# Kernel tuning notes

Measured on AMD Instinct MI355X. Metric: run time of the kernel, lower is better.

The kernel has to match this reference:

```python
import jax, jax.numpy as jnp
import numpy as np

N = 32768          # number of points
K = 64             # max_num_neighbors
D = 3              # spatial dim (3x3 local frames)
R = 1.0            # radius
TARGET_DEG = 48.0  # desired mean neighborhood size


def _radius_graph_numpy(pos, r, k):
    """Padded radius neighbor search (mimics torch_cluster.radius, incl. self-loop).

    Returns (edge_src, edge_dst, num_neighbors); padded slots have src == dst so
    edge_vec = 0 and they contribute nothing to the covariance scatter.
    """
    n = pos.shape[0]
    nbr = np.full((n, k), -1, dtype=np.int64)
    r2 = r * r
    chunk = 2048
    for s in range(0, n, chunk):
        q = pos[s:s + chunk]                                   # [C, D]
        d2 = ((q[:, None, :] - pos[None, :, :]) ** 2).sum(-1)  # [C, N]
        d2m = np.where(d2 <= r2, d2, np.inf)
        idx = np.argpartition(d2m, k - 1, axis=1)[:, :k]       # k nearest candidates
        dsel = np.take_along_axis(d2m, idx, axis=1)
        nbr[s:s + chunk] = np.where(np.isfinite(dsel), idx, -1)
    num_neighbors = (nbr >= 0).sum(axis=1).astype(np.int32)
    edge_dst = np.repeat(np.arange(n, dtype=np.int64), k)
    edge_src = nbr.reshape(-1)
    edge_src = np.where(edge_src >= 0, edge_src, edge_dst)     # pad: src == dst
    return edge_src.astype(np.int32), edge_dst.astype(np.int32), num_neighbors


def setup_inputs() -> dict:
    rng = np.random.default_rng(0)
    # box size so that density * (4/3) pi r^3 ~= TARGET_DEG
    L = (N * (4.0 / 3.0) * np.pi * R ** 3 / TARGET_DEG) ** (1.0 / 3.0)
    pos = rng.uniform(0.0, L, size=(N, D)).astype(np.float32)
    edge_src, edge_dst, num_neighbors = _radius_graph_numpy(pos, R, K)
    return {
        "pos": jnp.asarray(pos),
        "edge_src": jnp.asarray(edge_src),
        "edge_dst": jnp.asarray(edge_dst),
        "num_neighbors": jnp.asarray(num_neighbors),
    }


def reference(pos, edge_src, edge_dst, num_neighbors):
    n = pos.shape[0]
    # edge_vec = pos[col] - pos[row]; padded edges (src==dst) give exact zeros
    ev = pos[edge_src] - pos[edge_dst]                         # [E, 3]
    outer = ev[:, :, None] * ev[:, None, :]                    # [E, 3, 3]
    cov = jax.ops.segment_sum(outer, edge_dst, num_segments=n)  # [N, 3, 3]

    no_nbr = num_neighbors <= 1                                # self-loop only
    # replace degenerate (zero) covariances with a distinct-eigenvalue matrix so
    # eigh is well-defined; these rows are zeroed afterwards (exceptional 'zero').
    safe = jnp.diag(jnp.arange(1.0, D + 1.0, dtype=pos.dtype))
    cov = jnp.where(no_nbr[:, None, None], safe, cov)

    _, vecs = jnp.linalg.eigh(cov)                             # [N, 3, 3] columns = eigvecs
    frames = vecs.transpose(0, 2, 1)                           # rows = eigvecs
    frames = jnp.where(no_nbr[:, None, None], 0.0, frames)
    return frames


if __name__ == "__main__":
    out = reference(**setup_inputs())
    print(out.shape, out.dtype)
```

## Files before the change

### kernel.cpp

```cpp
#include <hip/hip_runtime.h>
#include <math.h>


#pragma clang fp contract(off)

#define EPS_F32    5.9604645e-8f
#define SAFMIN_F32 1.17549435e-38f

__device__ __forceinline__ float lapy2f(float x, float y) {
#pragma clang fp contract(off)
  float xa = fabsf(x), ya = fabsf(y);
  float w = fmaxf(xa, ya);
  float z = fminf(xa, ya);
  if (z == 0.0f) return w;
  float t = z / w;
  return w * sqrtf(1.0f + t * t);
}

__device__ __forceinline__ void slartgf(float f, float g, float* c, float* s, float* r) {
#pragma clang fp contract(off)
  const float safmin = SAFMIN_F32;
  const float safmax = 8.50705917e37f;
  const float rtmin  = 1.08420217e-19f;
  const float rtmax  = 6.52530446e18f;
  if (g == 0.0f) { *c = 1.0f; *s = 0.0f; *r = f; return; }
  if (f == 0.0f) { *c = 0.0f; *s = copysignf(1.0f, g); *r = fabsf(g); return; }
  float f1 = fabsf(f), g1 = fabsf(g);
  if (f1 > rtmin && f1 < rtmax && g1 > rtmin && g1 < rtmax) {
    float d = sqrtf(f * f + g * g);
    *c = f1 / d;
    *r = copysignf(d, f);
    *s = g / (*r);
  } else {
    float u  = fminf(safmax, fmaxf(safmin, fmaxf(f1, g1)));
    float fs = f / u, gs = g / u;
    float d  = sqrtf(fs * fs + gs * gs);
    *c = fabsf(fs) / d;
    float rr = copysignf(d, f);
    *s = gs / rr;
    *r = rr * u;
  }
}

__device__ __forceinline__ void slaev2f(float a, float b, float c,
                                        float* rt1, float* rt2,
                                        float* cs1, float* sn1) {
#pragma clang fp contract(off)
  float sm  = a + c;
  float df  = a - c;
  float adf = fabsf(df);
  float tb  = b + b;
  float ab  = fabsf(tb);
  float acmx, acmn;
  if (fabsf(a) > fabsf(c)) { acmx = a; acmn = c; } else { acmx = c; acmn = a; }
  float rt;
  if (adf > ab)      { float t = ab / adf; rt = adf * sqrtf(1.0f + t * t); }
  else if (adf < ab) { float t = adf / ab; rt = ab  * sqrtf(1.0f + t * t); }
  else               { rt = ab * sqrtf(2.0f); }
  int sgn1;
  if (sm < 0.0f) {
    *rt1 = 0.5f * (sm - rt); sgn1 = -1;
    *rt2 = (acmx / *rt1) * acmn - (b / *rt1) * b;
  } else if (sm > 0.0f) {
    *rt1 = 0.5f * (sm + rt); sgn1 = 1;
    *rt2 = (acmx / *rt1) * acmn - (b / *rt1) * b;
  } else {
    *rt1 = 0.5f * rt; *rt2 = -0.5f * rt; sgn1 = 1;
  }
  int sgn2; float cs;
  if (df >= 0.0f) { cs = df + rt; sgn2 = 1; }
  else            { cs = df - rt; sgn2 = -1; }
  float acs = fabsf(cs);
  if (acs > ab) {
    float ct = -tb / cs;
    *sn1 = 1.0f / sqrtf(1.0f + ct * ct);
    *cs1 = ct * (*sn1);
  } else {
    if (ab == 0.0f) { *cs1 = 1.0f; *sn1 = 0.0f; }
    else {
      float tn = -cs / tb;
      *cs1 = 1.0f / sqrtf(1.0f + tn * tn);
      *sn1 = tn * (*cs1);
    }
  }
  if (sgn1 == sgn2) { float tn = *cs1; *cs1 = -(*sn1); *sn1 = tn; }
}

__device__ void eig_frames_reg(float c00, float c01, float c02,
                               float c11, float c12, float c22,
                               float* __restrict__ o) {
#pragma clang fp contract(off)
  float d1, d2, d3, e1, e2, tau1, v2;
  {
    float a11 = c00, a21 = c01, a31 = c02, a22 = c11, a32 = c12, a33 = c22;
    float xnorm = fabsf(a31);
    if (xnorm == 0.0f) {
      tau1 = 0.0f; v2 = 0.0f;
      d1 = a11; d2 = a22; d3 = a33;
      e1 = a21; e2 = a32;
    } else {
      float py2  = lapy2f(a21, xnorm);
      float beta = -copysignf(py2, a21);
      tau1 = (beta - a21) / beta;
      v2   = a31 * (1.0f / (a21 - beta));
      float t2 = a32 * v2;
      float w1 = __builtin_fmaf(tau1, t2, tau1 * a22);
      float w2 = __builtin_fmaf(tau1 * v2, a33, tau1 * a32);
      float dot = __builtin_fmaf(v2, w2, w1);
      float ac = (-0.5f * tau1) * dot;
      w1 = w1 + ac;
      w2 = __builtin_fmaf(ac, v2, w2);
      float A11 = a22 - w1;
      A11 = A11 - w1;
      float A21 = a32 - w2;
      A21 = __builtin_fmaf(-w1, v2, A21);
      float A33 = __builtin_fmaf(-v2, w2, a33);
      A33 = __builtin_fmaf(-w2, v2, A33);
      d1 = a11; d2 = A11; d3 = A33;
      e1 = beta; e2 = A21;
    }
  }

  float z11 = 1.0f, z12 = 0.0f, z13 = 0.0f;
  float z21 = 0.0f, z22 = 1.0f, z23 = 0.0f;
  float z31 = 0.0f, z32 = 0.0f, z33 = 1.0f;
  float wc0, wc1, ws0, ws1;

#define DGET(i)    ((i) == 1 ? d1 : (i) == 2 ? d2 : d3)
#define DSET(i,v)  do { float _t = (v); if ((i) == 1) d1 = _t; else if ((i) == 2) d2 = _t; else d3 = _t; } while (0)
#define EGET(i)    ((i) == 1 ? e1 : e2)
#define ESET(i,v)  do { float _t = (v); if ((i) == 1) e1 = _t; else e2 = _t; } while (0)
#define ZGETC(r,c) ((r) == 1 ? ((c) == 1 ? z11 : (c) == 2 ? z12 : z13) \
                  : (r) == 2 ? ((c) == 1 ? z21 : (c) == 2 ? z22 : z23) \
                  :            ((c) == 1 ? z31 : (c) == 2 ? z32 : z33))
#define ZSETC(r,c,v) do { float _t = (v); \
    if ((r) == 1)      { if ((c) == 1) z11 = _t; else if ((c) == 2) z12 = _t; else z13 = _t; } \
    else if ((r) == 2) { if ((c) == 1) z21 = _t; else if ((c) == 2) z22 = _t; else z23 = _t; } \
    else               { if ((c) == 1) z31 = _t; else if ((c) == 2) z32 = _t; else z33 = _t; } } while (0)

  {
    const float eps    = EPS_F32;
    const float eps2   = eps * eps;
    const float safmin = SAFMIN_F32;
    const float ssfmax = sqrtf(8.50705917e37f) / 3.0f;
    const float ssfmin = sqrtf(safmin) / eps2;

    int   l1, l, m, lsv, lend, lendsv, iscale;
    const int nmaxit = 90;
    int   jtot = 0;
    float anorm, p, g, r, rt1, rt2, rc, rs, f, b, t;

    l1 = 1;

L10:
    if (l1 > 3) goto L160;
    if (l1 > 1) ESET(l1 - 1, 0.0f);
    if (l1 <= 2) {
      for (m = l1; m <= 2; m++) {
        float tst = fabsf(EGET(m));
        if (tst == 0.0f) goto L30;
        if (tst <= (sqrtf(fabsf(DGET(m))) * sqrtf(fabsf(DGET(m + 1)))) * eps) {
          ESET(m, 0.0f);
          goto L30;
        }
      }
    }
    m = 3;
L30:
    l = l1; lsv = l; lend = m; lendsv = lend; l1 = m + 1;
    if (lend == l) goto L10;

    anorm = 0.0f;
    for (int q = l; q <= lend; q++)     anorm = fmaxf(anorm, fabsf(DGET(q)));
    for (int q = l; q <= lend - 1; q++) anorm = fmaxf(anorm, fabsf(EGET(q)));
    iscale = 0;
    if (anorm == 0.0f) goto L10;
    if (anorm > ssfmax) {
      iscale = 1;
      float sc = ssfmax / anorm;
      for (int q = l; q <= lend; q++)     DSET(q, DGET(q) * sc);
      for (int q = l; q <= lend - 1; q++) ESET(q, EGET(q) * sc);
    } else if (anorm < ssfmin) {
      iscale = 2;
      float sc = ssfmin / anorm;
      for (int q = l; q <= lend; q++)     DSET(q, DGET(q) * sc);
      for (int q = l; q <= lend - 1; q++) ESET(q, EGET(q) * sc);
    }

    if (fabsf(DGET(lend)) < fabsf(DGET(l))) { lend = lsv; l = lendsv; }

    if (lend > l) {
L40:
      if (l != lend) {
        if (l == 1) {
          float tst = e1 * e1;
          if (tst <= (eps2 * fabsf(d1)) * fabsf(d2) + safmin) { m = 1; goto L60; }
        }
        if (lend == 3) {
          float tst = e2 * e2;
          if (tst <= (eps2 * fabsf(d2)) * fabsf(d3) + safmin) { m = 2; goto L60; }
        }
      }
      m = lend;
L60:
      if (m < lend) ESET(m, 0.0f);
      p = DGET(l);
      if (m == l) goto L80;
      if (m == l + 1) {
        if (l == 1) {
          slaev2f(d1, e1, d2, &rt1, &rt2, &rc, &rs);
          t = z12; z12 = rc * t - rs * z11; z11 = rs * t + rc * z11;
          t = z22; z22 = rc * t - rs * z21; z21 = rs * t + rc * z21;
          t = z32; z32 = rc * t - rs * z31; z31 = rs * t + rc * z31;
          d1 = rt1; d2 = rt2; e1 = 0.0f;
        } else {
          slaev2f(d2, e2, d3, &rt1, &rt2, &rc, &rs);
          t = z13; z13 = rc * t - rs * z12; z12 = rs * t + rc * z12;
          t = z23; z23 = rc * t - rs * z22; z22 = rs * t + rc * z22;
          t = z33; z33 = rc * t - rs * z32; z32 = rs * t + rc * z32;
          d2 = rt1; d3 = rt2; e2 = 0.0f;
        }
        l += 2;
        if (l <= lend) goto L40;
        goto L140;
      }
      if (jtot == nmaxit) goto L140;
      jtot++;
      g = (d2 - p) / (2.0f * e1);
      r = lapy2f(g, 1.0f);
      g = d3 - p + (e1 / (g + copysignf(r, g)));
      rs = 1.0f; rc = 1.0f; p = 0.0f;
      f = rs * e2;
      b = rc * e2;
      slartgf(g, f, &rc, &rs, &r);
      g = d3 - p;
      r = (d2 - g) * rs + 2.0f * rc * b;
      p = rs * r;
      d3 = g + p;
      g = rc * r - b;
      wc1 = rc; ws1 = -rs;
      f = rs * e1;
      b = rc * e1;
      slartgf(g, f, &rc, &rs, &r);
      e2 = r;
      g = d2 - p;
      r = (d1 - g) * rs + 2.0f * rc * b;
      p = rs * r;
      d2 = g + p;
      g = rc * r - b;
      wc0 = rc; ws0 = -rs;
      if (wc1 != 1.0f || ws1 != 0.0f) {
        t = z13; z13 = wc1 * t - ws1 * z12; z12 = ws1 * t + wc1 * z12;
        t = z23; z23 = wc1 * t - ws1 * z22; z22 = ws1 * t + wc1 * z22;
        t = z33; z33 = wc1 * t - ws1 * z32; z32 = ws1 * t + wc1 * z32;
      }
      if (wc0 != 1.0f || ws0 != 0.0f) {
        t = z12; z12 = wc0 * t - ws0 * z11; z11 = ws0 * t + wc0 * z11;
        t = z22; z22 = wc0 * t - ws0 * z21; z21 = ws0 * t + wc0 * z21;
        t = z32; z32 = wc0 * t - ws0 * z31; z31 = ws0 * t + wc0 * z31;
      }
      d1 = d1 - p;
      e1 = g;
      goto L40;
L80:
      DSET(l, p);
      l++;
      if (l <= lend) goto L40;
      goto L140;
    } else {
L90:
      if (l != lend) {
        if (l == 3) {
          float tst = e2 * e2;
          if (tst <= (eps2 * fabsf(d3)) * fabsf(d2) + safmin) { m = 3; goto L110; }
        }
        if (lend == 1) {
          float tst = e1 * e1;
          if (tst <= (eps2 * fabsf(d2)) * fabsf(d1) + safmin) { m = 2; goto L110; }
        }
      }
      m = lend;
L110:
      if (m > lend) ESET(m - 1, 0.0f);
      p = DGET(l);
      if (m == l) goto L130;
      if (m == l - 1) {
        if (l == 2) {
          slaev2f(d1, e1, d2, &rt1, &rt2, &rc, &rs);
          t = z12; z12 = rc * t - rs * z11; z11 = rs * t + rc * z11;
          t = z22; z22 = rc * t - rs * z21; z21 = rs * t + rc * z21;
          t = z32; z32 = rc * t - rs * z31; z31 = rs * t + rc * z31;
          d1 = rt1; d2 = rt2; e1 = 0.0f;
        } else {
          slaev2f(d2, e2, d3, &rt1, &rt2, &rc, &rs);
          t = z13; z13 = rc * t - rs * z12; z12 = rs * t + rc * z12;
          t = z23; z23 = rc * t - rs * z22; z22 = rs * t + rc * z22;
          t = z33; z33 = rc * t - rs * z32; z32 = rs * t + rc * z32;
          d2 = rt1; d3 = rt2; e2 = 0.0f;
        }
        l -= 2;
        if (l >= lend) goto L90;
        goto L140;
      }
      if (jtot == nmaxit) goto L140;
      jtot++;
      g = (d2 - p) / (2.0f * e2);
      r = lapy2f(g, 1.0f);
      g = d1 - p + (e2 / (g + copysignf(r, g)));
      rs = 1.0f; rc = 1.0f; p = 0.0f;
      f = rs * e1;
      b = rc * e1;
      slartgf(g, f, &rc, &rs, &r);
      g = d1 - p;
      r = (d2 - g) * rs + 2.0f * rc * b;
      p = rs * r;
      d1 = g + p;
      g = rc * r - b;
      wc0 = rc; ws0 = rs;
      f = rs * e2;
      b = rc * e2;
      slartgf(g, f, &rc, &rs, &r);
      e1 = r;
      g = d2 - p;
      r = (d3 - g) * rs + 2.0f * rc * b;
      p = rs * r;
      d2 = g + p;
      g = rc * r - b;
      wc1 = rc; ws1 = rs;
      if (wc0 != 1.0f || ws0 != 0.0f) {
        t = z12; z12 = wc0 * t - ws0 * z11; z11 = ws0 * t + wc0 * z11;
        t = z22; z22 = wc0 * t - ws0 * z21; z21 = ws0 * t + wc0 * z21;
        t = z32; z32 = wc0 * t - ws0 * z31; z31 = ws0 * t + wc0 * z31;
      }
      if (wc1 != 1.0f || ws1 != 0.0f) {
        t = z13; z13 = wc1 * t - ws1 * z12; z12 = ws1 * t + wc1 * z12;
        t = z23; z23 = wc1 * t - ws1 * z22; z22 = ws1 * t + wc1 * z22;
        t = z33; z33 = wc1 * t - ws1 * z32; z32 = ws1 * t + wc1 * z32;
      }
      d3 = d3 - p;
      e2 = g;
      goto L90;
L130:
      DSET(l, p);
      l--;
      if (l >= lend) goto L90;
      goto L140;
    }

L140:
    if (iscale == 1) {
      float sc = anorm / ssfmax;
      for (int q = lsv; q <= lendsv; q++)     DSET(q, DGET(q) * sc);
      for (int q = lsv; q <= lendsv - 1; q++) ESET(q, EGET(q) * sc);
    } else if (iscale == 2) {
      float sc = anorm / ssfmin;
      for (int q = lsv; q <= lendsv; q++)     DSET(q, DGET(q) * sc);
      for (int q = lsv; q <= lendsv - 1; q++) ESET(q, EGET(q) * sc);
    }
    if (jtot < nmaxit) goto L10;
    goto L160;

L160:
    for (int ii = 2; ii <= 3; ii++) {
      int i = ii - 1, kk = i;
      p = DGET(i);
      for (int j = ii; j <= 3; j++) {
        if (DGET(j) < p) { kk = j; p = DGET(j); }
      }
      if (kk != i) {
        DSET(kk, DGET(i));
        DSET(i, p);
        #pragma unroll
        for (int row = 1; row <= 3; row++) {
          float tt = ZGETC(row, i);
          ZSETC(row, i, ZGETC(row, kk));
          ZSETC(row, kk, tt);
        }
      }
    }
  }

#undef DGET
#undef DSET
#undef EGET
#undef ESET
#undef ZGETC
#undef ZSETC

  if (tau1 != 0.0f) {
    {
      float z2 = z21, z3 = z31;
      float w = z2 + z3 * v2;
      float t = tau1 * w;
      z21 = __builtin_fmaf(-tau1, w, z2);
      z31 = __builtin_fmaf(v2, -t, z3);
    }
    {
      float z2 = z22, z3 = z32;
      float w = z2 + z3 * v2;
      float t = tau1 * w;
      z22 = __builtin_fmaf(-tau1, w, z2);
      z32 = __builtin_fmaf(v2, -t, z3);
    }
    {
      float z2 = z23, z3 = z33;
      float w = z2 + z3 * v2;
      float t = tau1 * w;
      z23 = __builtin_fmaf(-tau1, w, z2);
      z33 = __builtin_fmaf(v2, -t, z3);
    }
  }

  o[0] = z11; o[1] = z21; o[2] = z31;
  o[3] = z12; o[4] = z22; o[5] = z32;
  o[6] = z13; o[7] = z23; o[8] = z33;
}

#define NODES_PER_BLOCK 64
#define NODE_STRIDE     193

struct __attribute__((aligned(4))) f3 { float x, y, z; };

__global__ void __launch_bounds__(256)
pca_frames_tiled_kernel(const float* __restrict__ pos,
                        const int*   __restrict__ esrc,
                        const int*   __restrict__ nn,
                        float*       __restrict__ out,
                        int n)
{
#pragma clang fp contract(off)
  __shared__ float sev[NODES_PER_BLOCK * NODE_STRIDE];

  const int tid   = threadIdx.x;
  const int node0 = blockIdx.x * NODES_PER_BLOCK;

  const int ebase = blockIdx.x * (NODES_PER_BLOCK * 64);
  #pragma unroll
  for (int q = 0; q < (NODES_PER_BLOCK * 64) / 256; ++q) {
    int eb  = q * 256 + tid;
    int n_b = eb >> 6;
    int j   = eb & 63;
    int i   = node0 + n_b;
    int s   = esrc[ebase + eb];
    f3 ps   = *reinterpret_cast<const f3*>(pos + 3 * s);
    float dx = ps.x - pos[3 * i + 0];
    float dy = ps.y - pos[3 * i + 1];
    float dz = ps.z - pos[3 * i + 2];
    float* row = sev + n_b * NODE_STRIDE + 3 * j;
    row[0] = dx;
    row[1] = dy;
    row[2] = dz;
  }

  __syncthreads();

  if (tid < 64) {
    int i = node0 + tid;
    float* o = out + (size_t)i * 9;

    if (nn[i] <= 1) {
      #pragma unroll
      for (int j = 0; j < 9; ++j) o[j] = 0.0f;
      return;
    }

    const float* row = sev + tid * NODE_STRIDE;
    float c00 = 0.0f, c01 = 0.0f, c02 = 0.0f, c11 = 0.0f, c12 = 0.0f, c22 = 0.0f;
    for (int j = 0; j < 64; ++j) {
      float dx = row[3 * j + 0];
      float dy = row[3 * j + 1];
      float dz = row[3 * j + 2];
      c00 = c00 + dx * dx;
      c01 = c01 + dx * dy;
      c02 = c02 + dx * dz;
      c11 = c11 + dy * dy;
      c12 = c12 + dy * dz;
      c22 = c22 + dz * dz;
    }

    eig_frames_reg(c00, c01, c02, c11, c12, c22, o);
  }
}

__global__ void __launch_bounds__(64)
pca_frames_fused_kernel(const float* __restrict__ pos,
                        const int*   __restrict__ esrc,
                        const int*   __restrict__ nn,
                        float*       __restrict__ out,
                        int n, int k)
{
#pragma clang fp contract(off)
  int i = blockIdx.x * blockDim.x + threadIdx.x;
  if (i >= n) return;
  float* o = out + (size_t)i * 9;

  if (nn[i] <= 1) {
    #pragma unroll
    for (int j = 0; j < 9; ++j) o[j] = 0.0f;
    return;
  }

  float px = pos[3 * i + 0], py = pos[3 * i + 1], pz = pos[3 * i + 2];
  float c00 = 0.0f, c01 = 0.0f, c02 = 0.0f, c11 = 0.0f, c12 = 0.0f, c22 = 0.0f;
  const int* ep = esrc + (size_t)i * k;
  for (int j = 0; j < k; ++j) {
    int sidx = ep[j];
    float dx = pos[3 * sidx + 0] - px;
    float dy = pos[3 * sidx + 1] - py;
    float dz = pos[3 * sidx + 2] - pz;
    c00 = c00 + dx * dx;
    c01 = c01 + dx * dy;
    c02 = c02 + dx * dz;
    c11 = c11 + dy * dy;
    c12 = c12 + dy * dz;
    c22 = c22 + dz * dz;
  }

  eig_frames_reg(c00, c01, c02, c11, c12, c22, o);
}

extern "C" void kernel_launch(void* const* d_in, const int* in_sizes, int n_in,
                              void* d_out, int out_size, void* d_ws, size_t ws_size,
                              hipStream_t stream) {
  const float* pos  = (const float*)d_in[0];
  const int*   esrc = (const int*)d_in[1];
  const int*   nn   = (const int*)d_in[3];
  float*       out  = (float*)d_out;

  int n = in_sizes[0] / 3;
  if (n <= 0) return;
  int k = in_sizes[1] / n;

  if (k == 64 && (n % NODES_PER_BLOCK) == 0) {
    hipLaunchKernelGGL(pca_frames_tiled_kernel, dim3(n / NODES_PER_BLOCK),
                       dim3(256), 0, stream, pos, esrc, nn, out, n);
  } else {
    const int block = 64;
    hipLaunchKernelGGL(pca_frames_fused_kernel, dim3((n + block - 1) / block),
                       dim3(block), 0, stream, pos, esrc, nn, out, n, k);
  }
}
```

Before: 95.36 us.

## Restructure QL/QR eigen iteration as a wave-uniform state machine to cut divergence

Replaces the goto-based LAPACK ssteqr port with an explicit state machine looping until no lane in the wavefront is active. The QL and QR branches are merged into one sweep body by index mirroring (dirQL), so lanes that take different directions now run the same code instead of serialised divergent paths. The cost is extra selects, per-iteration __any wave votes, and register pressure from the mirrored indexing.

```diff
diff --git a/kernel.cpp b/kernel.cpp
--- a/kernel.cpp
+++ b/kernel.cpp
@@ -86,9 +86,17 @@
   if (sgn1 == sgn2) { float tn = *cs1; *cs1 = -(*sn1); *sn1 = tn; }
 }
 
-__device__ void eig_frames_reg(float c00, float c01, float c02,
-                               float c11, float c12, float c22,
-                               float* __restrict__ o) {
+#define ST_SEG   0
+#define ST_CHK   1
+#define ST_X21   2
+#define ST_X32   3
+#define ST_SWP   4
+#define ST_RESC  5
+#define ST_DONE  6
+
+__device__ void eig_frames_sm(float c00, float c01, float c02,
+                              float c11, float c12, float c22,
+                              float* __restrict__ o) {
 #pragma clang fp contract(off)
   float d1, d2, d3, e1, e2, tau1, v2;
   {
@@ -124,12 +132,15 @@
   float z11 = 1.0f, z12 = 0.0f, z13 = 0.0f;
   float z21 = 0.0f, z22 = 1.0f, z23 = 0.0f;
   float z31 = 0.0f, z32 = 0.0f, z33 = 1.0f;
-  float wc0, wc1, ws0, ws1;
 
 #define DGET(i)    ((i) == 1 ? d1 : (i) == 2 ? d2 : d3)
 #define DSET(i,v)  do { float _t = (v); if ((i) == 1) d1 = _t; else if ((i) == 2) d2 = _t; else d3 = _t; } while (0)
 #define EGET(i)    ((i) == 1 ? e1 : e2)
 #define ESET(i,v)  do { float _t = (v); if ((i) == 1) e1 = _t; else e2 = _t; } while (0)
+#define AGET(i)    DGET(dirQL ? (i) : 4 - (i))
+#define ASET(i,v)  DSET(dirQL ? (i) : 4 - (i), v)
+#define BGET(i)    EGET(dirQL ? (i) : 3 - (i))
+#define BSET(i,v)  ESET(dirQL ? (i) : 3 - (i), v)
 #define ZGETC(r,c) ((r) == 1 ? ((c) == 1 ? z11 : (c) == 2 ? z12 : z13) \
                   : (r) == 2 ? ((c) == 1 ? z21 : (c) == 2 ? z22 : z23) \
                   :            ((c) == 1 ? z31 : (c) == 2 ? z32 : z33))
@@ -138,229 +149,217 @@
     else if ((r) == 2) { if ((c) == 1) z21 = _t; else if ((c) == 2) z22 = _t; else z23 = _t; } \
     else               { if ((c) == 1) z31 = _t; else if ((c) == 2) z32 = _t; else z33 = _t; } } while (0)
 
+  const float eps    = EPS_F32;
+  const float eps2   = eps * eps;
+  const float safmin = SAFMIN_F32;
+  const float ssfmax = sqrtf(8.50705917e37f) / 3.0f;
+  const float ssfmin = sqrtf(safmin) / eps2;
+  const int   nmaxit = 90;
+
+  int   st = ST_SEG, nst = ST_CHK;
+  int   l1 = 1, lm = 1, lendm = 1, lsv = 1, lendsv = 1, iscale = 0, jtot = 0;
+  bool  dirQL = true;
+  float anorm = 0.0f, p = 0.0f;
+
+  for (int it = 0; it < 600; ++it) {
+    if (!__any(st != ST_DONE)) break;
+
+    if (st == ST_SEG) {
+      for (int pass = 0; pass < 4 && st == ST_SEG; ++pass) {
+        if (l1 > 3) { st = ST_DONE; break; }
+        if (l1 > 1) ESET(l1 - 1, 0.0f);
+        int m = 3;
+        {
+          bool found = false;
+          if (l1 <= 2) {
+            for (int mi = l1; mi <= 2 && !found; mi++) {
+              float tst = fabsf(EGET(mi));
+              if (tst == 0.0f) { m = mi; found = true; }
+              else if (tst <= (sqrtf(fabsf(DGET(mi))) * sqrtf(fabsf(DGET(mi + 1)))) * eps) {
+                ESET(mi, 0.0f); m = mi; found = true;
+              }
+            }
+          }
+        }
+        int l = l1; lsv = l; int lend = m; lendsv = lend; l1 = m + 1;
+        if (lend == l) continue;
+        anorm = 0.0f;
+        for (int q = l; q <= lend; q++)     anorm = fmaxf(anorm, fabsf(DGET(q)));
+        for (int q = l; q <= lend - 1; q++) anorm = fmaxf(anorm, fabsf(EGET(q)));
+        iscale = 0;
+        if (anorm == 0.0f) continue;
+        if (anorm > ssfmax) {
+          iscale = 1;
+          float sc = ssfmax / anorm;
+          for (int q = l; q <= lend; q++)     DSET(q, DGET(q) * sc);
+          for (int q = l; q <= lend - 1; q++) ESET(q, EGET(q) * sc);
+        } else if (anorm < ssfmin) {
+          iscale = 2;
+          float sc = ssfmin / anorm;
+          for (int q = l; q <= lend; q++)     DSET(q, DGET(q) * sc);
+          for (int q = l; q <= lend - 1; q++) ESET(q, EGET(q) * sc);
+        }
+        if (fabsf(DGET(lend)) < fabsf(DGET(l))) { int tt = l; l = lend; lend = tt; }
+        dirQL = (lend > l);
+        lm    = dirQL ? l : 4 - l;
+        lendm = dirQL ? lend : 4 - lend;
+        st = ST_CHK;
+      }
+    }
+
+    if (st == ST_CHK) {
+      int mm = lendm;
+      {
+        bool found = false;
+        if (lm != lendm) {
+          if (lm == 1) {
+            float bb = BGET(1);
+            float tst = bb * bb;
+            if (tst <= (eps2 * fabsf(AGET(1))) * fabsf(AGET(2)) + safmin) { mm = 1; found = true; }
+          }
+          if (!found && lendm == 3) {
+            float bb = BGET(2);
+            float tst = bb * bb;
+            if (tst <= (eps2 * fabsf(AGET(2))) * fabsf(AGET(3)) + safmin) { mm = 2; found = true; }
+          }
+        }
+      }
+      if (mm < lendm) BSET(mm, 0.0f);
+      p = AGET(lm);
+      if (mm == lm) {
+        ASET(lm, p); lm++;
+        st = (lm <= lendm) ? ST_CHK : ST_RESC;
+      } else if (mm == lm + 1) {
+        int lo = dirQL ? lm : 4 - mm;
+        lm += 2;
+        nst = (lm <= lendm) ? ST_CHK : ST_RESC;
+        st = (lo == 1) ? ST_X21 : ST_X32;
+      } else {
+        st = (jtot == nmaxit) ? ST_RESC : ST_SWP;
+      }
+    }
+
+    if (st == ST_X21) {
+      float rt1, rt2, rc, rs, t;
+      slaev2f(d1, e1, d2, &rt1, &rt2, &rc, &rs);
+      t = z12; z12 = rc * t - rs * z11; z11 = rs * t + rc * z11;
+      t = z22; z22 = rc * t - rs * z21; z21 = rs * t + rc * z21;
+      t = z32; z32 = rc * t - rs * z31; z31 = rs * t + rc * z31;
+      d1 = rt1; d2 = rt2; e1 = 0.0f;
+      st = nst;
+    }
+
+    if (st == ST_X32) {
+      float rt1, rt2, rc, rs, t;
+      slaev2f(d2, e2, d3, &rt1, &rt2, &rc, &rs);
+      t = z13; z13 = rc * t - rs * z12; z12 = rs * t + rc * z12;
+      t = z23; z23 = rc * t - rs * z22; z22 = rs * t + rc * z22;
+      t = z33; z33 = rc * t - rs * z32; z32 = rs * t + rc * z32;
+      d2 = rt1; d3 = rt2; e2 = 0.0f;
+      st = nst;
+    }
+
+    if (st == ST_SWP) {
+      jtot++;
+      float a1 = dirQL ? d1 : d3;
+      float a2 = d2;
+      float a3 = dirQL ? d3 : d1;
+      float b1 = dirQL ? e1 : e2;
+      float b2 = dirQL ? e2 : e1;
+      float g, r, rc, rs, f, b;
+      g = (a2 - p) / (2.0f * b1);
+      r = lapy2f(g, 1.0f);
+      g = a3 - p + (b1 / (g + copysignf(r, g)));
+      rs = 1.0f; rc = 1.0f; p = 0.0f;
+      f = rs * b2;
+      b = rc * b2;
+      slartgf(g, f, &rc, &rs, &r);
+      g = a3 - p;
+      r = (a2 - g) * rs + 2.0f * rc * b;
+      p = rs * r;
+      a3 = g + p;
+      g = rc * r - b;
+      float wcA = rc, rsA = rs;
+      f = rs * b1;
+      b = rc * b1;
+      slartgf(g, f, &rc, &rs, &r);
+      b2 = r;
+      g = a2 - p;
+      r = (a1 - g) * rs + 2.0f * rc * b;
+      p = rs * r;
+      a2 = g + p;
+      g = rc * r - b;
+      float wcB = rc, rsB = rs;
+      if (wcA != 1.0f || rsA != 0.0f) {
+        {
+          float hi = dirQL ? z13 : z11, lo = z12;
+          float nh = wcA * hi + rsA * lo;
+          float nl = wcA * lo - rsA * hi;
+          if (dirQL) z13 = nh; else z11 = nh;
+          z12 = nl;
+        }
+        {
+          float hi = dirQL ? z23 : z21, lo = z22;
+          float nh = wcA * hi + rsA * lo;
+          float nl = wcA * lo - rsA * hi;
+          if (dirQL) z23 = nh; else z21 = nh;
+          z22 = nl;
+        }
+        {
+          float hi = dirQL ? z33 : z31, lo = z32;
+          float nh = wcA * hi + rsA * lo;
+          float nl = wcA * lo - rsA * hi;
+          if (dirQL) z33 = nh; else z31 = nh;
+          z32 = nl;
+        }
+      }
+      if (wcB != 1.0f || rsB != 0.0f) {
+        {
+          float hi = z12, lo = dirQL ? z11 : z13;
+          float nh = wcB * hi + rsB * lo;
+          float nl = wcB * lo - rsB * hi;
+          z12 = nh;
+          if (dirQL) z11 = nl; else z13 = nl;
+        }
+        {
+          float hi = z22, lo = dirQL ? z21 : z23;
+          float nh = wcB * hi + rsB * lo;
+          float nl = wcB * lo - rsB * hi;
+          z22 = nh;
+          if (dirQL) z21 = nl; else z23 = nl;
+        }
+        {
+          float hi = z32, lo = dirQL ? z31 : z33;
+          float nh = wcB * hi + rsB * lo;
+          float nl = wcB * lo - rsB * hi;
+          z32 = nh;
+          if (dirQL) z31 = nl; else z33 = nl;
+        }
+      }
+      a1 = a1 - p;
+      b1 = g;
+      if (dirQL) { d1 = a1; d3 = a3; e1 = b1; e2 = b2; }
+      else       { d3 = a1; d1 = a3; e2 = b1; e1 = b2; }
+      d2 = a2;
+      st = ST_CHK;
+    }
+
+    if (st == ST_RESC) {
+      if (iscale == 1) {
+        float sc = anorm / ssfmax;
+        for (int q = lsv; q <= lendsv; q++)     DSET(q, DGET(q) * sc);
+        for (int q = lsv; q <= lendsv - 1; q++) ESET(q, EGET(q) * sc);
+      } else if (iscale == 2) {
+        float sc = anorm / ssfmin;
+        for (int q = lsv; q <= lendsv; q++)     DSET(q, DGET(q) * sc);
+        for (int q = lsv; q <= lendsv - 1; q++) ESET(q, EGET(q) * sc);
+      }
+      st = (jtot < nmaxit) ? ST_SEG : ST_DONE;
+    }
+  }
+
   {
-    const float eps    = EPS_F32;
-    const float eps2   = eps * eps;
-    const float safmin = SAFMIN_F32;
-    const float ssfmax = sqrtf(8.50705917e37f) / 3.0f;
-    const float ssfmin = sqrtf(safmin) / eps2;
-
-    int   l1, l, m, lsv, lend, lendsv, iscale;
-    const int nmaxit = 90;
-    int   jtot = 0;
-    float anorm, p, g, r, rt1, rt2, rc, rs, f, b, t;
-
-    l1 = 1;
-
-L10:
-    if (l1 > 3) goto L160;
-    if (l1 > 1) ESET(l1 - 1, 0.0f);
-    if (l1 <= 2) {
-      for (m = l1; m <= 2; m++) {
-        float tst = fabsf(EGET(m));
-        if (tst == 0.0f) goto L30;
-        if (tst <= (sqrtf(fabsf(DGET(m))) * sqrtf(fabsf(DGET(m + 1)))) * eps) {
-          ESET(m, 0.0f);
-          goto L30;
-        }
-      }
-    }
-    m = 3;
-L30:
-    l = l1; lsv = l; lend = m; lendsv = lend; l1 = m + 1;
-    if (lend == l) goto L10;
-
-    anorm = 0.0f;
-    for (int q = l; q <= lend; q++)     anorm = fmaxf(anorm, fabsf(DGET(q)));
-    for (int q = l; q <= lend - 1; q++) anorm = fmaxf(anorm, fabsf(EGET(q)));
-    iscale = 0;
-    if (anorm == 0.0f) goto L10;
-    if (anorm > ssfmax) {
-      iscale = 1;
-      float sc = ssfmax / anorm;
-      for (int q = l; q <= lend; q++)     DSET(q, DGET(q) * sc);
-      for (int q = l; q <= lend - 1; q++) ESET(q, EGET(q) * sc);
-    } else if (anorm < ssfmin) {
-      iscale = 2;
-      float sc = ssfmin / anorm;
-      for (int q = l; q <= lend; q++)     DSET(q, DGET(q) * sc);
-      for (int q = l; q <= lend - 1; q++) ESET(q, EGET(q) * sc);
-    }
-
-    if (fabsf(DGET(lend)) < fabsf(DGET(l))) { lend = lsv; l = lendsv; }
-
-    if (lend > l) {
-L40:
-      if (l != lend) {
-        if (l == 1) {
-          float tst = e1 * e1;
-          if (tst <= (eps2 * fabsf(d1)) * fabsf(d2) + safmin) { m = 1; goto L60; }
-        }
-        if (lend == 3) {
-          float tst = e2 * e2;
-          if (tst <= (eps2 * fabsf(d2)) * fabsf(d3) + safmin) { m = 2; goto L60; }
-        }
-      }
-      m = lend;
-L60:
-      if (m < lend) ESET(m, 0.0f);
-      p = DGET(l);
-      if (m == l) goto L80;
-      if (m == l + 1) {
-        if (l == 1) {
-          slaev2f(d1, e1, d2, &rt1, &rt2, &rc, &rs);
-          t = z12; z12 = rc * t - rs * z11; z11 = rs * t + rc * z11;
-          t = z22; z22 = rc * t - rs * z21; z21 = rs * t + rc * z21;
-          t = z32; z32 = rc * t - rs * z31; z31 = rs * t + rc * z31;
-          d1 = rt1; d2 = rt2; e1 = 0.0f;
-        } else {
-          slaev2f(d2, e2, d3, &rt1, &rt2, &rc, &rs);
-          t = z13; z13 = rc * t - rs * z12; z12 = rs * t + rc * z12;
-          t = z23; z23 = rc * t - rs * z22; z22 = rs * t + rc * z22;
-          t = z33; z33 = rc * t - rs * z32; z32 = rs * t + rc * z32;
-          d2 = rt1; d3 = rt2; e2 = 0.0f;
-        }
-        l += 2;
-        if (l <= lend) goto L40;
-        goto L140;
-      }
-      if (jtot == nmaxit) goto L140;
-      jtot++;
-      g = (d2 - p) / (2.0f * e1);
-      r = lapy2f(g, 1.0f);
-      g = d3 - p + (e1 / (g + copysignf(r, g)));
-      rs = 1.0f; rc = 1.0f; p = 0.0f;
-      f = rs * e2;
-      b = rc * e2;
-      slartgf(g, f, &rc, &rs, &r);
-      g = d3 - p;
-      r = (d2 - g) * rs + 2.0f * rc * b;
-      p = rs * r;
-      d3 = g + p;
-      g = rc * r - b;
-      wc1 = rc; ws1 = -rs;
-      f = rs * e1;
-      b = rc * e1;
-      slartgf(g, f, &rc, &rs, &r);
-      e2 = r;
-      g = d2 - p;
-      r = (d1 - g) * rs + 2.0f * rc * b;
-      p = rs * r;
-      d2 = g + p;
-      g = rc * r - b;
-      wc0 = rc; ws0 = -rs;
-      if (wc1 != 1.0f || ws1 != 0.0f) {
-        t = z13; z13 = wc1 * t - ws1 * z12; z12 = ws1 * t + wc1 * z12;
-        t = z23; z23 = wc1 * t - ws1 * z22; z22 = ws1 * t + wc1 * z22;
-        t = z33; z33 = wc1 * t - ws1 * z32; z32 = ws1 * t + wc1 * z32;
-      }
-      if (wc0 != 1.0f || ws0 != 0.0f) {
-        t = z12; z12 = wc0 * t - ws0 * z11; z11 = ws0 * t + wc0 * z11;
-        t = z22; z22 = wc0 * t - ws0 * z21; z21 = ws0 * t + wc0 * z21;
-        t = z32; z32 = wc0 * t - ws0 * z31; z31 = ws0 * t + wc0 * z31;
-      }
-      d1 = d1 - p;
-      e1 = g;
-      goto L40;
-L80:
-      DSET(l, p);
-      l++;
-      if (l <= lend) goto L40;
-      goto L140;
-    } else {
-L90:
-      if (l != lend) {
-        if (l == 3) {
-          float tst = e2 * e2;
-          if (tst <= (eps2 * fabsf(d3)) * fabsf(d2) + safmin) { m = 3; goto L110; }
-        }
-        if (lend == 1) {
-          float tst = e1 * e1;
-          if (tst <= (eps2 * fabsf(d2)) * fabsf(d1) + safmin) { m = 2; goto L110; }
-        }
-      }
-      m = lend;
-L110:
-      if (m > lend) ESET(m - 1, 0.0f);
-      p = DGET(l);
-      if (m == l) goto L130;
-      if (m == l - 1) {
-        if (l == 2) {
-          slaev2f(d1, e1, d2, &rt1, &rt2, &rc, &rs);
-          t = z12; z12 = rc * t - rs * z11; z11 = rs * t + rc * z11;
-          t = z22; z22 = rc * t - rs * z21; z21 = rs * t + rc * z21;
-          t = z32; z32 = rc * t - rs * z31; z31 = rs * t + rc * z31;
-          d1 = rt1; d2 = rt2; e1 = 0.0f;
-        } else {
-          slaev2f(d2, e2, d3, &rt1, &rt2, &rc, &rs);
-          t = z13; z13 = rc * t - rs * z12; z12 = rs * t + rc * z12;
-          t = z23; z23 = rc * t - rs * z22; z22 = rs * t + rc * z22;
-          t = z33; z33 = rc * t - rs * z32; z32 = rs * t + rc * z32;
-          d2 = rt1; d3 = rt2; e2 = 0.0f;
-        }
-        l -= 2;
-        if (l >= lend) goto L90;
-        goto L140;
-      }
-      if (jtot == nmaxit) goto L140;
-      jtot++;
-      g = (d2 - p) / (2.0f * e2);
-      r = lapy2f(g, 1.0f);
-      g = d1 - p + (e2 / (g + copysignf(r, g)));
-      rs = 1.0f; rc = 1.0f; p = 0.0f;
-      f = rs * e1;
-      b = rc * e1;
-      slartgf(g, f, &rc, &rs, &r);
-      g = d1 - p;
-      r = (d2 - g) * rs + 2.0f * rc * b;
-      p = rs * r;
-      d1 = g + p;
-      g = rc * r - b;
-      wc0 = rc; ws0 = rs;
-      f = rs * e2;
-      b = rc * e2;
-      slartgf(g, f, &rc, &rs, &r);
-      e1 = r;
-      g = d2 - p;
-      r = (d3 - g) * rs + 2.0f * rc * b;
-      p = rs * r;
-      d2 = g + p;
-      g = rc * r - b;
-      wc1 = rc; ws1 = rs;
-      if (wc0 != 1.0f || ws0 != 0.0f) {
-        t = z12; z12 = wc0 * t - ws0 * z11; z11 = ws0 * t + wc0 * z11;
-        t = z22; z22 = wc0 * t - ws0 * z21; z21 = ws0 * t + wc0 * z21;
-        t = z32; z32 = wc0 * t - ws0 * z31; z31 = ws0 * t + wc0 * z31;
-      }
-      if (wc1 != 1.0f || ws1 != 0.0f) {
-        t = z13; z13 = wc1 * t - ws1 * z12; z12 = ws1 * t + wc1 * z12;
-        t = z23; z23 = wc1 * t - ws1 * z22; z22 = ws1 * t + wc1 * z22;
-        t = z33; z33 = wc1 * t - ws1 * z32; z32 = ws1 * t + wc1 * z32;
-      }
-      d3 = d3 - p;
-      e2 = g;
-      goto L90;
-L130:
-      DSET(l, p);
-      l--;
-      if (l >= lend) goto L90;
-      goto L140;
-    }
-
-L140:
-    if (iscale == 1) {
-      float sc = anorm / ssfmax;
-      for (int q = lsv; q <= lendsv; q++)     DSET(q, DGET(q) * sc);
-      for (int q = lsv; q <= lendsv - 1; q++) ESET(q, EGET(q) * sc);
-    } else if (iscale == 2) {
-      float sc = anorm / ssfmin;
-      for (int q = lsv; q <= lendsv; q++)     DSET(q, DGET(q) * sc);
-      for (int q = lsv; q <= lendsv - 1; q++) ESET(q, EGET(q) * sc);
-    }
-    if (jtot < nmaxit) goto L10;
-    goto L160;
-
-L160:
+    float p;
     for (int ii = 2; ii <= 3; ii++) {
       int i = ii - 1, kk = i;
       p = DGET(i);
@@ -384,6 +383,10 @@
 #undef DSET
 #undef EGET
 #undef ESET
+#undef AGET
+#undef ASET
+#undef BGET
+#undef BSET
 #undef ZGETC
 #undef ZSETC
 
@@ -478,7 +481,7 @@
       c22 = c22 + dz * dz;
     }
 
-    eig_frames_reg(c00, c01, c02, c11, c12, c22, o);
+    eig_frames_sm(c00, c01, c02, c11, c12, c22, o);
   }
 }
 
@@ -516,7 +519,7 @@
     c22 = c22 + dz * dz;
   }
 
-  eig_frames_reg(c00, c01, c02, c11, c12, c22, o);
+  eig_frames_sm(c00, c01, c02, c11, c12, c22, o);
 }
 
 extern "C" void kernel_launch(void* const* d_in, const int* in_sizes, int n_in,
```

Result: faster. 89.57 us (-6.1%).
